# Performance work log

Measured on AMD Instinct MI355X. Metric: run time of the kernel, lower is better.

Reference implementation:

```python
import jax, jax.numpy as jnp
import numpy as np
from jax import lax

NUM_CLASSES = 9
IMG_H, IMG_W = 384, 640
SCORE_TH = 0.05
NMS_TH = 0.5
DET_PER_IMG = 100
PRE_NMS_K = 512  # pre-NMS top-k candidates per image (fixed-shape surrogate for nonzero())
BBOX_XFORM_CLIP = float(np.log(1000.0 / 16.0))
WX, WY, WW, WH = 10.0, 10.0, 5.0, 5.0
MIN_SIZE = 0.01


def _conv(x, w, padding):
    return lax.conv_general_dilated(x, w, (1, 1), padding,
                                    dimension_numbers=('NCHW', 'OIHW', 'NCHW'))


def _pairwise_iou(a, b):
    # a [K,4], b [K,4] -> [K,K]
    area_a = (a[:, 2] - a[:, 0]) * (a[:, 3] - a[:, 1])
    area_b = (b[:, 2] - b[:, 0]) * (b[:, 3] - b[:, 1])
    lt = jnp.maximum(a[:, None, :2], b[None, :, :2])
    rb = jnp.minimum(a[:, None, 2:], b[None, :, 2:])
    wh = jnp.clip(rb - lt, 0.0)
    inter = wh[..., 0] * wh[..., 1]
    return inter / jnp.maximum(area_a[:, None] + area_b[None, :] - inter, 1e-8)


def setup_inputs() -> dict:
    key = jax.random.key(0)
    ks = jax.random.split(key, 12)
    B, P, C_in = 2, 512, 512
    feats = jax.random.normal(ks[0], (B * P, C_in, 7, 7), jnp.float32)
    # well-formed proposal boxes inside the image
    cx = jax.random.uniform(ks[1], (B, P)) * IMG_W
    cy = jax.random.uniform(ks[2], (B, P)) * IMG_H
    w = jax.random.uniform(ks[3], (B, P)) * 100.0 + 8.0
    h = jax.random.uniform(ks[4], (B, P)) * 100.0 + 8.0
    proposals = jnp.stack([cx - w / 2, cy - h / 2, cx + w / 2, cy + h / 2], -1)
    w1 = jax.random.normal(ks[5], (1024, C_in, 3, 3), jnp.float32) * 0.02
    w2 = jax.random.normal(ks[6], (1024, 1024, 3, 3), jnp.float32) * 0.02
    wd = jax.random.normal(ks[7], (1024, C_in, 1, 1), jnp.float32) * 0.02
    cls_w = jax.random.normal(ks[8], (NUM_CLASSES, 1024), jnp.float32) * 0.02
    cls_b = jnp.zeros((NUM_CLASSES,), jnp.float32)
    reg_w = jax.random.normal(ks[9], (NUM_CLASSES * 4, 1024), jnp.float32) * 0.02
    reg_b = jnp.zeros((NUM_CLASSES * 4,), jnp.float32)
    return dict(instance_features=feats, proposals=proposals, w1=w1, w2=w2, wd=wd,
                cls_w=cls_w, cls_b=cls_b, reg_w=reg_w, reg_b=reg_b)


def _per_image(boxes, scores):
    # boxes [P, C, 4], scores [P, C]
    P = boxes.shape[0]
    b = boxes[:, 1:].reshape(-1, 4)                 # drop background class
    s = scores[:, 1:].reshape(-1)
    lab = jnp.broadcast_to(jnp.arange(1, NUM_CLASSES), (P, NUM_CLASSES - 1)).reshape(-1)
    ws = b[:, 2] - b[:, 0]
    hs = b[:, 3] - b[:, 1]
    valid = (s > SCORE_TH) & (ws >= MIN_SIZE) & (hs >= MIN_SIZE)
    s = jnp.where(valid, s, -jnp.inf)
    s_top, idx = lax.top_k(s, PRE_NMS_K)            # sorted descending -> greedy NMS order
    b_top = b[idx]
    lab_top = lab[idx]
    # class-aware NMS via per-class coordinate offset (batched_nms trick)
    off = lab_top.astype(b.dtype)[:, None] * (float(max(IMG_H, IMG_W)) + 1.0)
    iou = _pairwise_iou(b_top + off, b_top + off)
    keep0 = jnp.isfinite(s_top)
    ar = jnp.arange(PRE_NMS_K)

    def body(i, keep):
        sup = (iou[i] > NMS_TH) & (ar > i) & keep[i]
        return keep & ~sup

    keep = lax.fori_loop(0, PRE_NMS_K, body, keep0)
    ks = jnp.where(keep, s_top, -jnp.inf)
    fs, fidx = lax.top_k(ks, DET_PER_IMG)
    fb = b_top[fidx]
    fl = lab_top[fidx]
    fvalid = jnp.isfinite(fs)
    return (jnp.where(fvalid[:, None], fb, 0.0),
            jnp.where(fvalid, fs, 0.0),
            jnp.where(fvalid, fl, 0),
            fvalid)


def reference(instance_features, proposals, w1, w2, wd, cls_w, cls_b, reg_w, reg_b):
    B, P = proposals.shape[0], proposals.shape[1]
    x = instance_features
    # Residual_Basic: two 3x3 convs + 1x1 downsample shortcut, relu
    h = jax.nn.relu(_conv(x, w1, 'SAME'))
    h = _conv(h, w2, 'SAME')
    embedded = jax.nn.relu(h + _conv(x, wd, 'VALID'))          # [N,1024,7,7]
    flat = embedded.mean(axis=(2, 3))                          # AdaptiveAvgPool2d(1)+Flatten
    cls_scores = flat @ cls_w.T + cls_b                        # [N, C]
    bbox_reg = flat @ reg_w.T + reg_b                          # [N, 4C]

    # ---- box decode (BoxCoder weights (10,10,5,5)) ----
    props = proposals.reshape(-1, 4)
    pw = props[:, 2] - props[:, 0]
    ph = props[:, 3] - props[:, 1]
    pcx = props[:, 0] + 0.5 * pw
    pcy = props[:, 1] + 0.5 * ph
    rel = bbox_reg.reshape(-1, NUM_CLASSES, 4)
    dx = rel[..., 0] / WX
    dy = rel[..., 1] / WY
    dw = jnp.minimum(rel[..., 2] / WW, BBOX_XFORM_CLIP)
    dh = jnp.minimum(rel[..., 3] / WH, BBOX_XFORM_CLIP)
    ncx = dx * pw[:, None] + pcx[:, None]
    ncy = dy * ph[:, None] + pcy[:, None]
    nw = jnp.exp(dw) * pw[:, None]
    nh = jnp.exp(dh) * ph[:, None]
    pred_boxes = jnp.stack([ncx - 0.5 * nw, ncy - 0.5 * nh,
                            ncx + 0.5 * nw, ncy + 0.5 * nh], -1)  # [N,C,4]
    # clip to image
    pred_boxes = jnp.stack([
        jnp.clip(pred_boxes[..., 0], 0.0, IMG_W),
        jnp.clip(pred_boxes[..., 1], 0.0, IMG_H),
        jnp.clip(pred_boxes[..., 2], 0.0, IMG_W),
        jnp.clip(pred_boxes[..., 3], 0.0, IMG_H)], -1)
    pred_scores = jax.nn.softmax(cls_scores, -1)

    det_boxes, det_scores, det_labels, det_valid = jax.vmap(_per_image)(
        pred_boxes.reshape(B, P, NUM_CLASSES, 4),
        pred_scores.reshape(B, P, NUM_CLASSES))
    return embedded, cls_scores, bbox_reg, det_boxes, det_scores, det_labels, det_valid
```

## Files before the change

kernel.cpp:

```cpp
#include <hip/hip_runtime.h>
#include <math.h>

#define N_IMG 1024
#define C_IN 512
#define C_MID 1024
#define HW 7
#define SP 49
#define NCOLS (N_IMG*SP)
#define LDSROW 40

typedef short bf16x8 __attribute__((ext_vector_type(8)));
typedef float f32x4  __attribute__((ext_vector_type(4)));

__device__ __forceinline__ unsigned splitpack(float v) {
    unsigned u  = __float_as_uint(v);
    unsigned hi = (u + 0x7FFFu + ((u >> 16) & 1u)) >> 16;
    float hf    = __uint_as_float(hi << 16);
    float d     = v - hf;
    unsigned ud = __float_as_uint(d);
    unsigned lo = (ud + 0x7FFFu + ((ud >> 16) & 1u)) >> 16;
    return (hi & 0xFFFFu) | (lo << 16);
}

__global__ __launch_bounds__(256)
void pack_x(const float* __restrict__ X, unsigned* __restrict__ Xpk)
{
    int i = blockIdx.x*256 + threadIdx.x;
    Xpk[i] = splitpack(X[i]);
}

__global__ __launch_bounds__(256)
void pack_w1(const float* __restrict__ w, unsigned short* __restrict__ Wh,
             unsigned short* __restrict__ Wl)
{
    int e = blockIdx.x*256 + threadIdx.x;
    int cp = e & 31, oc = (e>>5)&127, bm = (e>>12)&7, cc = (e>>15)&15, r = e>>19;
    float v = w[((size_t)(bm*128+oc)*512 + (cc*32+cp))*9 + r];
    unsigned pk = splitpack(v);
    Wh[e] = (unsigned short)(pk & 0xFFFFu);
    Wl[e] = (unsigned short)(pk >> 16);
}
__global__ __launch_bounds__(256)
void pack_w2(const float* __restrict__ w, unsigned short* __restrict__ Wh,
             unsigned short* __restrict__ Wl)
{
    int e = blockIdx.x*256 + threadIdx.x;
    int cp = e & 31, oc = (e>>5)&127, bm = (e>>12)&7, cc = (e>>15)&31, r = e>>20;
    float v = w[((size_t)(bm*128+oc)*1024 + (cc*32+cp))*9 + r];
    unsigned pk = splitpack(v);
    Wh[e] = (unsigned short)(pk & 0xFFFFu);
    Wl[e] = (unsigned short)(pk >> 16);
}
__global__ __launch_bounds__(256)
void pack_wd(const float* __restrict__ w, unsigned short* __restrict__ Wh,
             unsigned short* __restrict__ Wl)
{
    int e = blockIdx.x*256 + threadIdx.x;
    int cp = e & 31, oc = (e>>5)&127, bm = (e>>12)&7, cc = e>>15;
    float v = w[(size_t)(bm*128+oc)*512 + cc*32+cp];
    unsigned pk = splitpack(v);
    Wh[e] = (unsigned short)(pk & 0xFFFFu);
    Wl[e] = (unsigned short)(pk >> 16);
}

template<int MODE>
__global__ __launch_bounds__(256)
void conv_mfma(const unsigned* __restrict__ Bpk,
               const float* __restrict__ Xf,
               const unsigned short* __restrict__ Wh,
               const unsigned short* __restrict__ Wl,
               const unsigned short* __restrict__ Dh,
               const unsigned short* __restrict__ Dl,
               float* __restrict__ outF, unsigned* __restrict__ outU)
{
    constexpr int CS  = MODE ? C_MID : C_IN;
    constexpr int NCC = MODE ? 32 : 16;
    __shared__ unsigned short As_hi[128*LDSROW];
    __shared__ unsigned short As_lo[128*LDSROW];
    __shared__ unsigned short Bs_hi[128*LDSROW];
    __shared__ unsigned short Bs_lo[128*LDSROW];

    const int tid = threadIdx.x;
    const int bn = blockIdx.x, bm = blockIdx.y;

    const int ln = tid & 63;
    const int wv = tid >> 6;
    const int lm = ln & 15, lq = ln >> 4;
    const int wm = (wv & 1) * 64;
    const int wn = (wv >> 1) * 64;
    const int koff = lq * 8;

    const int aoff = (tid >> 1)*LDSROW + (tid & 1)*16;
    const int bcol = tid >> 1;
    const int half16 = (tid & 1) * 16;
    const int col = bn*128 + bcol;
    const int bnimg = col / SP;
    const int bp = col - bnimg*SP;
    const int by = bp / HW;
    const int bx = bp - by*HW;
    const int bo = bcol*LDSROW + half16;

    f32x4 acc[4][4];
    #pragma unroll
    for (int i = 0; i < 4; i++)
        #pragma unroll
        for (int j = 0; j < 4; j++)
            acc[i][j] = (f32x4){0.f, 0.f, 0.f, 0.f};

    for (int r = 0; r < 9; ++r) {
        const int t3 = r / 3;
        const int dy = t3 - 1;
        const int dx = (r - t3*3) - 1;
        const bool valid = ((unsigned)(by + dy) < (unsigned)HW) &&
                           ((unsigned)(bx + dx) < (unsigned)HW);
        const int pp = bp + dy*HW + dx;
        for (int cc = 0; cc < NCC; ++cc) {
            {
                const size_t tb = ((size_t)((r*NCC + cc)*8 + bm) << 12) + tid*16;
                uint4 h0 = *(const uint4*)(Wh + tb);
                uint4 h1 = *(const uint4*)(Wh + tb + 8);
                uint4 l0 = *(const uint4*)(Wl + tb);
                uint4 l1 = *(const uint4*)(Wl + tb + 8);
                *(uint4*)&As_hi[aoff]     = h0;
                *(uint4*)&As_hi[aoff + 8] = h1;
                *(uint4*)&As_lo[aoff]     = l0;
                *(uint4*)&As_lo[aoff + 8] = l1;
            }
            {
                unsigned v[16];
                if (valid) {
                    const unsigned* src =
                        Bpk + ((size_t)bnimg*CS + cc*32 + half16)*SP + pp;
                    #pragma unroll
                    for (int e = 0; e < 16; ++e) v[e] = src[e*SP];
                } else {
                    #pragma unroll
                    for (int e = 0; e < 16; ++e) v[e] = 0u;
                }
                unsigned hp[8], lp[8];
                #pragma unroll
                for (int j2 = 0; j2 < 8; ++j2) {
                    unsigned p0 = v[2*j2], p1 = v[2*j2+1];
                    hp[j2] = (p0 & 0xFFFFu) | (p1 << 16);
                    lp[j2] = (p0 >> 16) | (p1 & 0xFFFF0000u);
                }
                *(uint4*)&Bs_hi[bo]     = *(uint4*)&hp[0];
                *(uint4*)&Bs_hi[bo + 8] = *(uint4*)&hp[4];
                *(uint4*)&Bs_lo[bo]     = *(uint4*)&lp[0];
                *(uint4*)&Bs_lo[bo + 8] = *(uint4*)&lp[4];
            }
            __syncthreads();
            {
                bf16x8 ah[4], bh[4], al[4], bl[4];
                #pragma unroll
                for (int i = 0; i < 4; i++)
                    ah[i] = *(const bf16x8*)&As_hi[(wm + i*16 + lm)*LDSROW + koff];
                #pragma unroll
                for (int j = 0; j < 4; j++)
                    bh[j] = *(const bf16x8*)&Bs_hi[(wn + j*16 + lm)*LDSROW + koff];
                #pragma unroll
                for (int i = 0; i < 4; i++)
                    #pragma unroll
                    for (int j = 0; j < 4; j++)
                        acc[i][j] = __builtin_amdgcn_mfma_f32_16x16x32_bf16(
                            ah[i], bh[j], acc[i][j], 0, 0, 0);
                #pragma unroll
                for (int i = 0; i < 4; i++)
                    al[i] = *(const bf16x8*)&As_lo[(wm + i*16 + lm)*LDSROW + koff];
                #pragma unroll
                for (int i = 0; i < 4; i++)
                    #pragma unroll
                    for (int j = 0; j < 4; j++)
                        acc[i][j] = __builtin_amdgcn_mfma_f32_16x16x32_bf16(
                            al[i], bh[j], acc[i][j], 0, 0, 0);
                #pragma unroll
                for (int j = 0; j < 4; j++)
                    bl[j] = *(const bf16x8*)&Bs_lo[(wn + j*16 + lm)*LDSROW + koff];
                #pragma unroll
                for (int i = 0; i < 4; i++)
                    #pragma unroll
                    for (int j = 0; j < 4; j++)
                        acc[i][j] = __builtin_amdgcn_mfma_f32_16x16x32_bf16(
                            ah[i], bl[j], acc[i][j], 0, 0, 0);
            }
            __syncthreads();
        }
    }
    if (MODE == 1) {
        for (int cc = 0; cc < 16; ++cc) {
            {
                const size_t tb = ((size_t)(cc*8 + bm) << 12) + tid*16;
                uint4 h0 = *(const uint4*)(Dh + tb);
                uint4 h1 = *(const uint4*)(Dh + tb + 8);
                uint4 l0 = *(const uint4*)(Dl + tb);
                uint4 l1 = *(const uint4*)(Dl + tb + 8);
                *(uint4*)&As_hi[aoff]     = h0;
                *(uint4*)&As_hi[aoff + 8] = h1;
                *(uint4*)&As_lo[aoff]     = l0;
                *(uint4*)&As_lo[aoff + 8] = l1;
            }
            {
                const float* src = Xf + ((size_t)bnimg*C_IN + cc*32 + half16)*SP + bp;
                unsigned v[16];
                #pragma unroll
                for (int e = 0; e < 16; ++e) v[e] = splitpack(src[e*SP]);
                unsigned hp[8], lp[8];
                #pragma unroll
                for (int j2 = 0; j2 < 8; ++j2) {
                    unsigned p0 = v[2*j2], p1 = v[2*j2+1];
                    hp[j2] = (p0 & 0xFFFFu) | (p1 << 16);
                    lp[j2] = (p0 >> 16) | (p1 & 0xFFFF0000u);
                }
                *(uint4*)&Bs_hi[bo]     = *(uint4*)&hp[0];
                *(uint4*)&Bs_hi[bo + 8] = *(uint4*)&hp[4];
                *(uint4*)&Bs_lo[bo]     = *(uint4*)&lp[0];
                *(uint4*)&Bs_lo[bo + 8] = *(uint4*)&lp[4];
            }
            __syncthreads();
            {
                bf16x8 ah[4], bh[4], al[4], bl[4];
                #pragma unroll
                for (int i = 0; i < 4; i++)
                    ah[i] = *(const bf16x8*)&As_hi[(wm + i*16 + lm)*LDSROW + koff];
                #pragma unroll
                for (int j = 0; j < 4; j++)
                    bh[j] = *(const bf16x8*)&Bs_hi[(wn + j*16 + lm)*LDSROW + koff];
                #pragma unroll
                for (int i = 0; i < 4; i++)
                    #pragma unroll
                    for (int j = 0; j < 4; j++)
                        acc[i][j] = __builtin_amdgcn_mfma_f32_16x16x32_bf16(
                            ah[i], bh[j], acc[i][j], 0, 0, 0);
                #pragma unroll
                for (int i = 0; i < 4; i++)
                    al[i] = *(const bf16x8*)&As_lo[(wm + i*16 + lm)*LDSROW + koff];
                #pragma unroll
                for (int i = 0; i < 4; i++)
                    #pragma unroll
                    for (int j = 0; j < 4; j++)
                        acc[i][j] = __builtin_amdgcn_mfma_f32_16x16x32_bf16(
                            al[i], bh[j], acc[i][j], 0, 0, 0);
                #pragma unroll
                for (int j = 0; j < 4; j++)
                    bl[j] = *(const bf16x8*)&Bs_lo[(wn + j*16 + lm)*LDSROW + koff];
                #pragma unroll
                for (int i = 0; i < 4; i++)
                    #pragma unroll
                    for (int j = 0; j < 4; j++)
                        acc[i][j] = __builtin_amdgcn_mfma_f32_16x16x32_bf16(
                            ah[i], bl[j], acc[i][j], 0, 0, 0);
            }
            __syncthreads();
        }
    }

    #pragma unroll
    for (int j = 0; j < 4; j++) {
        const int gc = bn*128 + wn + j*16 + lm;
        const int n = gc / SP;
        const int p = gc - n*SP;
        #pragma unroll
        for (int i = 0; i < 4; i++) {
            #pragma unroll
            for (int r = 0; r < 4; r++) {
                const int m = bm*128 + wm + i*16 + lq*4 + r;
                float val = fmaxf(acc[i][j][r], 0.f);
                if (MODE == 0)
                    outU[((size_t)n*C_MID + m)*SP + p] = splitpack(val);
                else
                    outF[((size_t)n*C_MID + m)*SP + p] = val;
            }
        }
    }
}

__global__ __launch_bounds__(256)
void pool_kernel(const float* __restrict__ emb, float* __restrict__ flat)
{
    int n = blockIdx.x;
    for (int c = threadIdx.x; c < C_MID; c += 256) {
        const float* p = emb + ((size_t)n*C_MID + c)*SP;
        float s = 0.f;
        #pragma unroll
        for (int i = 0; i < SP; i++) s += p[i];
        flat[n*C_MID + c] = s / 49.0f;
    }
}

__global__ __launch_bounds__(64)
void head_kernel(const float* __restrict__ flat,
                 const float* __restrict__ cls_w, const float* __restrict__ cls_b,
                 const float* __restrict__ reg_w, const float* __restrict__ reg_b,
                 const float* __restrict__ props,
                 float* __restrict__ cls_out, float* __restrict__ reg_out,
                 float* __restrict__ pbox, float* __restrict__ pscore)
{
    int n = blockIdx.x;
    __shared__ float f[C_MID];
    __shared__ float logits[9];
    __shared__ float regs[36];
    for (int c = threadIdx.x; c < C_MID; c += 64) f[c] = flat[n*C_MID + c];
    __syncthreads();
    int o = threadIdx.x;
    if (o < 45) {
        const float* w = (o < 9) ? (cls_w + o*C_MID) : (reg_w + (o-9)*C_MID);
        float a = (o < 9) ? cls_b[o] : reg_b[o-9];
        for (int c = 0; c < C_MID; c++) a = fmaf(f[c], w[c], a);
        if (o < 9) { cls_out[n*9 + o] = a; logits[o] = a; }
        else       { reg_out[n*36 + (o-9)] = a; regs[o-9] = a; }
    }
    __syncthreads();
    if (o < 9) {
        float m = logits[0];
        for (int i = 1; i < 9; i++) m = fmaxf(m, logits[i]);
        float se = 0.f;
        for (int i = 0; i < 9; i++) se += expf(logits[i] - m);
        pscore[n*9 + o] = expf(logits[o] - m) / se;
        {
            #pragma clang fp contract(off)
            float x1 = props[n*4+0], y1 = props[n*4+1];
            float x2 = props[n*4+2], y2 = props[n*4+3];
            float pw = x2 - x1, ph = y2 - y1;
            float pcx = x1 + 0.5f*pw, pcy = y1 + 0.5f*ph;
            float dx = regs[o*4+0] / 10.0f;
            float dy = regs[o*4+1] / 10.0f;
            float dw = fminf(regs[o*4+2] / 5.0f, 4.135166556742356f);
            float dh = fminf(regs[o*4+3] / 5.0f, 4.135166556742356f);
            float ncx = dx*pw + pcx, ncy = dy*ph + pcy;
            float nw = expf(dw)*pw,  nh = expf(dh)*ph;
            float bx1 = ncx - 0.5f*nw, by1 = ncy - 0.5f*nh;
            float bx2 = ncx + 0.5f*nw, by2 = ncy + 0.5f*nh;
            bx1 = fminf(fmaxf(bx1, 0.f), 640.f);
            by1 = fminf(fmaxf(by1, 0.f), 384.f);
            bx2 = fminf(fmaxf(bx2, 0.f), 640.f);
            by2 = fminf(fmaxf(by2, 0.f), 384.f);
            float* dst = pbox + (n*9 + o)*4;
            dst[0] = bx1; dst[1] = by1; dst[2] = bx2; dst[3] = by2;
        }
    }
}

__global__ __launch_bounds__(1024)
void nms_kernel(const float* __restrict__ pbox, const float* __restrict__ pscore,
                float* __restrict__ dbox, float* __restrict__ dsc,
                float* __restrict__ dlab, float* __restrict__ dval)
{
    #pragma clang fp contract(off)
    const int b = blockIdx.x;
    const int tid = threadIdx.x;
    __shared__ unsigned long long mbuf[4096];
    __shared__ float s512[512];
    __shared__ int   id512[512];
    __shared__ float obx[512][4];
    __shared__ unsigned long long keepw[8];
    float* sc = (float*)mbuf;
    int*   si = (int*)(sc + 4096);
    const float NEG_INF = -__builtin_inff();

    for (int i = tid; i < 4096; i += 1024) {
        int p = i >> 3;
        int c = (i & 7) + 1;
        int n = b*512 + p;
        float s = pscore[n*9 + c];
        const float* bb = pbox + (n*9 + c)*4;
        float w = bb[2] - bb[0], h = bb[3] - bb[1];
        bool valid = (s > 0.05f) && (w >= 0.01f) && (h >= 0.01f);
        sc[i] = valid ? s : NEG_INF;
        si[i] = i;
    }
    __syncthreads();
    for (int k = 2; k <= 4096; k <<= 1) {
        for (int j = k >> 1; j > 0; j >>= 1) {
            for (int i = tid; i < 4096; i += 1024) {
                int ixj = i ^ j;
                if (ixj > i) {
                    float s1 = sc[i], s2 = sc[ixj];
                    int i1 = si[i], i2 = si[ixj];
                    bool before12 = (s1 > s2) || ((s1 == s2) && (i1 < i2));
                    bool up = ((i & k) == 0);
                    if (up ? !before12 : before12) {
                        sc[i] = s2; sc[ixj] = s1;
                        si[i] = i2; si[ixj] = i1;
                    }
                }
            }
            __syncthreads();
        }
    }
    if (tid < 512) {
        float s = sc[tid];
        int id = si[tid];
        s512[tid] = s;
        id512[tid] = id;
        int c = (id & 7) + 1;
        int n = b*512 + (id >> 3);
        float off = (float)c * 641.0f;
        const float* bb = pbox + (n*9 + c)*4;
        obx[tid][0] = bb[0] + off;
        obx[tid][1] = bb[1] + off;
        obx[tid][2] = bb[2] + off;
        obx[tid][3] = bb[3] + off;
    }
    __syncthreads();
    unsigned long long* mask = mbuf;
    for (int idx = tid; idx < 4096; idx += 1024) {
        int i = idx >> 3, w = idx & 7;
        float ax1 = obx[i][0], ay1 = obx[i][1], ax2 = obx[i][2], ay2 = obx[i][3];
        float aarea = (ax2 - ax1) * (ay2 - ay1);
        unsigned long long m = 0;
        int j0 = w << 6;
        for (int jj = 0; jj < 64; jj++) {
            int j = j0 + jj;
            if (j > i) {
                float bx1 = obx[j][0], by1 = obx[j][1];
                float bx2 = obx[j][2], by2 = obx[j][3];
                float barea = (bx2 - bx1) * (by2 - by1);
                float lx = fmaxf(ax1, bx1), ly = fmaxf(ay1, by1);
                float rx = fminf(ax2, bx2), ry = fminf(ay2, by2);
                float iw = fmaxf(rx - lx, 0.f), ih = fmaxf(ry - ly, 0.f);
                float inter = iw * ih;
                float iou = inter / fmaxf(aarea + barea - inter, 1e-8f);
                if (iou > 0.5f) m |= (1ull << jj);
            }
        }
        mask[(i << 3) + w] = m;
    }
    if (tid < 8) {
        unsigned long long kw = 0;
        for (int jj = 0; jj < 64; jj++)
            if (s512[(tid << 6) + jj] != NEG_INF) kw |= (1ull << jj);
        keepw[tid] = kw;
    }
    __syncthreads();
    if (tid == 0) {
        for (int i = 0; i < 512; i++) {
            if ((keepw[i >> 6] >> (i & 63)) & 1ull) {
                const unsigned long long* mi = mask + (i << 3);
                #pragma unroll
                for (int w = 0; w < 8; w++) keepw[w] &= ~mi[w];
            }
        }
        int cnt = 0;
        for (int i = 0; i < 512 && cnt < 100; i++) {
            if ((keepw[i >> 6] >> (i & 63)) & 1ull) {
                int id = id512[i];
                int c = (id & 7) + 1;
                int n = b*512 + (id >> 3);
                const float* bb = pbox + (n*9 + c)*4;
                float* db = dbox + (b*100 + cnt)*4;
                db[0] = bb[0]; db[1] = bb[1]; db[2] = bb[2]; db[3] = bb[3];
                dsc[b*100 + cnt] = s512[i];
                dlab[b*100 + cnt] = (float)c;
                dval[b*100 + cnt] = 1.0f;
                cnt++;
            }
        }
        for (; cnt < 100; cnt++) {
            float* db = dbox + (b*100 + cnt)*4;
            db[0] = 0.f; db[1] = 0.f; db[2] = 0.f; db[3] = 0.f;
            dsc[b*100 + cnt] = 0.f;
            dlab[b*100 + cnt] = 0.f;
            dval[b*100 + cnt] = 0.f;
        }
    }
}

extern "C" void kernel_launch(void* const* d_in, const int* in_sizes, int n_in,
                              void* d_out, int out_size, void* d_ws, size_t ws_size,
                              hipStream_t stream)
{
    const float* X      = (const float*)d_in[0];
    const float* props  = (const float*)d_in[1];
    const float* w1     = (const float*)d_in[2];
    const float* w2     = (const float*)d_in[3];
    const float* wd     = (const float*)d_in[4];
    const float* cls_w  = (const float*)d_in[5];
    const float* cls_b  = (const float*)d_in[6];
    const float* reg_w  = (const float*)d_in[7];
    const float* reg_b  = (const float*)d_in[8];

    float* out     = (float*)d_out;
    float* emb     = out;
    float* cls_out = out + 51380224;
    float* reg_out = cls_out + 9216;
    float* dbox    = reg_out + 36864;
    float* dsc     = dbox + 800;
    float* dlab    = dsc + 200;
    float* dval    = dlab + 200;

    unsigned* Xpk            = (unsigned*)out;
    unsigned short* Wpk1h    = (unsigned short*)(out + 25690112);
    unsigned short* Wpk1l    = (unsigned short*)(out + 30408704);

    char* wsb = (char*)d_ws;
    unsigned* h_u         = (unsigned*)(wsb);
    unsigned short* Wpk2h = (unsigned short*)(wsb + 205520896);
    unsigned short* Wpk2l = (unsigned short*)(wsb + 224395264);
    unsigned short* Wpkdh = (unsigned short*)(wsb + 243269632);
    unsigned short* Wpkdl = (unsigned short*)(wsb + 244318208);
    float* flat           = (float*)(wsb + 245366784);
    float* pbox           = (float*)(wsb + 249561088);
    float* pscore         = (float*)(wsb + 249708544);

    pack_x <<<100352, 256, 0, stream>>>(X, Xpk);
    pack_w1<<<18432,  256, 0, stream>>>(w1, Wpk1h, Wpk1l);
    pack_w2<<<36864,  256, 0, stream>>>(w2, Wpk2h, Wpk2l);
    pack_wd<<<2048,   256, 0, stream>>>(wd, Wpkdh, Wpkdl);

    dim3 cgrid(NCOLS/128, C_MID/128);
    conv_mfma<0><<<cgrid, 256, 0, stream>>>(Xpk, X, Wpk1h, Wpk1l,
                                            nullptr, nullptr, nullptr, h_u);
    conv_mfma<1><<<cgrid, 256, 0, stream>>>(h_u, X, Wpk2h, Wpk2l,
                                            Wpkdh, Wpkdl, emb, nullptr);
    pool_kernel<<<N_IMG, 256, 0, stream>>>(emb, flat);
    head_kernel<<<N_IMG, 64, 0, stream>>>(flat, cls_w, cls_b, reg_w, reg_b, props,
                                          cls_out, reg_out, pbox, pscore);
    nms_kernel<<<2, 1024, 0, stream>>>(pbox, pscore, dbox, dsc, dlab, dval);
}
```

Before: 5.930 ms.

## Load conv weight tiles via direct global-to-LDS DMA and swap grid order

Weight tiles for the A operand are now copied straight into LDS with global_load_lds 16-byte transfers instead of going through registers. The A tile uses an unpadded 32-element row stride so the DMA layout matches. The grid is also transposed so adjacent blocks share the same column tile (the B activations) across the 8 output-channel blocks, which should improve L2 reuse of the gathered inputs. Risks: the unpadded A rows can cause LDS bank conflicts on the fragment reads, and the DMA must complete before the barrier (no explicit vmcnt wait is shown).

New measurement: 5.534 ms. 1.07x faster.

```diff
diff --git a/kernel.cpp b/kernel.cpp
--- a/kernel.cpp
+++ b/kernel.cpp
@@ -8,9 +8,16 @@
 #define SP 49
 #define NCOLS (N_IMG*SP)
 #define LDSROW 40
+#define AROW 32
 
 typedef short bf16x8 __attribute__((ext_vector_type(8)));
 typedef float f32x4  __attribute__((ext_vector_type(4)));
+
+__device__ __forceinline__ void dma16(const void* g, void* l) {
+    __builtin_amdgcn_global_load_lds(
+        (const __attribute__((address_space(1))) void*)g,
+        (__attribute__((address_space(3))) void*)l, 16, 0, 0);
+}
 
 __device__ __forceinline__ unsigned splitpack(float v) {
     unsigned u  = __float_as_uint(v);
@@ -75,13 +82,13 @@
 {
     constexpr int CS  = MODE ? C_MID : C_IN;
     constexpr int NCC = MODE ? 32 : 16;
-    __shared__ unsigned short As_hi[128*LDSROW];
-    __shared__ unsigned short As_lo[128*LDSROW];
-    __shared__ unsigned short Bs_hi[128*LDSROW];
-    __shared__ unsigned short Bs_lo[128*LDSROW];
+    __shared__ __align__(16) unsigned short As_hi[128*AROW];
+    __shared__ __align__(16) unsigned short As_lo[128*AROW];
+    __shared__ __align__(16) unsigned short Bs_hi[128*LDSROW];
+    __shared__ __align__(16) unsigned short Bs_lo[128*LDSROW];
 
     const int tid = threadIdx.x;
-    const int bn = blockIdx.x, bm = blockIdx.y;
+    const int bm = blockIdx.x, bn = blockIdx.y;
 
     const int ln = tid & 63;
     const int wv = tid >> 6;
@@ -90,7 +97,8 @@
     const int wn = (wv >> 1) * 64;
     const int koff = lq * 8;
 
-    const int aoff = (tid >> 1)*LDSROW + (tid & 1)*16;
+    const int go = wv*1024 + ln*8;
+
     const int bcol = tid >> 1;
     const int half16 = (tid & 1) * 16;
     const int col = bn*128 + bcol;
@@ -116,15 +124,11 @@
         const int pp = bp + dy*HW + dx;
         for (int cc = 0; cc < NCC; ++cc) {
             {
-                const size_t tb = ((size_t)((r*NCC + cc)*8 + bm) << 12) + tid*16;
-                uint4 h0 = *(const uint4*)(Wh + tb);
-                uint4 h1 = *(const uint4*)(Wh + tb + 8);
-                uint4 l0 = *(const uint4*)(Wl + tb);
-                uint4 l1 = *(const uint4*)(Wl + tb + 8);
-                *(uint4*)&As_hi[aoff]     = h0;
-                *(uint4*)&As_hi[aoff + 8] = h1;
-                *(uint4*)&As_lo[aoff]     = l0;
-                *(uint4*)&As_lo[aoff + 8] = l1;
+                const size_t tb = ((size_t)((r*NCC + cc)*8 + bm) << 12);
+                dma16(Wh + tb + go,       &As_hi[wv*1024]);
+                dma16(Wh + tb + go + 512, &As_hi[wv*1024 + 512]);
+                dma16(Wl + tb + go,       &As_lo[wv*1024]);
+                dma16(Wl + tb + go + 512, &As_lo[wv*1024 + 512]);
             }
             {
                 unsigned v[16];
@@ -154,7 +158,7 @@
                 bf16x8 ah[4], bh[4], al[4], bl[4];
                 #pragma unroll
                 for (int i = 0; i < 4; i++)
-                    ah[i] = *(const bf16x8*)&As_hi[(wm + i*16 + lm)*LDSROW + koff];
+                    ah[i] = *(const bf16x8*)&As_hi[(wm + i*16 + lm)*AROW + koff];
                 #pragma unroll
                 for (int j = 0; j < 4; j++)
                     bh[j] = *(const bf16x8*)&Bs_hi[(wn + j*16 + lm)*LDSROW + koff];
@@ -166,7 +170,7 @@
                             ah[i], bh[j], acc[i][j], 0, 0, 0);
                 #pragma unroll
                 for (int i = 0; i < 4; i++)
-                    al[i] = *(const bf16x8*)&As_lo[(wm + i*16 + lm)*LDSROW + koff];
+                    al[i] = *(const bf16x8*)&As_lo[(wm + i*16 + lm)*AROW + koff];
                 #pragma unroll
                 for (int i = 0; i < 4; i++)
                     #pragma unroll
@@ -189,15 +193,11 @@
     if (MODE == 1) {
         for (int cc = 0; cc < 16; ++cc) {
             {
-                const size_t tb = ((size_t)(cc*8 + bm) << 12) + tid*16;
-                uint4 h0 = *(const uint4*)(Dh + tb);
-                uint4 h1 = *(const uint4*)(Dh + tb + 8);
-                uint4 l0 = *(const uint4*)(Dl + tb);
-                uint4 l1 = *(const uint4*)(Dl + tb + 8);
-                *(uint4*)&As_hi[aoff]     = h0;
-                *(uint4*)&As_hi[aoff + 8] = h1;
-                *(uint4*)&As_lo[aoff]     = l0;
-                *(uint4*)&As_lo[aoff + 8] = l1;
+                const size_t tb = ((size_t)(cc*8 + bm) << 12);
+                dma16(Dh + tb + go,       &As_hi[wv*1024]);
+                dma16(Dh + tb + go + 512, &As_hi[wv*1024 + 512]);
+                dma16(Dl + tb + go,       &As_lo[wv*1024]);
+                dma16(Dl + tb + go + 512, &As_lo[wv*1024 + 512]);
             }
             {
                 const float* src = Xf + ((size_t)bnimg*C_IN + cc*32 + half16)*SP + bp;
@@ -221,7 +221,7 @@
                 bf16x8 ah[4], bh[4], al[4], bl[4];
                 #pragma unroll
                 for (int i = 0; i < 4; i++)
-                    ah[i] = *(const bf16x8*)&As_hi[(wm + i*16 + lm)*LDSROW + koff];
+                    ah[i] = *(const bf16x8*)&As_hi[(wm + i*16 + lm)*AROW + koff];
                 #pragma unroll
                 for (int j = 0; j < 4; j++)
                     bh[j] = *(const bf16x8*)&Bs_hi[(wn + j*16 + lm)*LDSROW + koff];
@@ -233,7 +233,7 @@
                             ah[i], bh[j], acc[i][j], 0, 0, 0);
                 #pragma unroll
                 for (int i = 0; i < 4; i++)
-                    al[i] = *(const bf16x8*)&As_lo[(wm + i*16 + lm)*LDSROW + koff];
+                    al[i] = *(const bf16x8*)&As_lo[(wm + i*16 + lm)*AROW + koff];
                 #pragma unroll
                 for (int i = 0; i < 4; i++)
                     #pragma unroll
@@ -507,7 +507,7 @@
     pack_w2<<<36864,  256, 0, stream>>>(w2, Wpk2h, Wpk2l);
     pack_wd<<<2048,   256, 0, stream>>>(wd, Wpkdh, Wpkdl);
 
-    dim3 cgrid(NCOLS/128, C_MID/128);
+    dim3 cgrid(C_MID/128, NCOLS/128);
     conv_mfma<0><<<cgrid, 256, 0, stream>>>(Xpk, X, Wpk1h, Wpk1l,
                                             nullptr, nullptr, nullptr, h_u);
     conv_mfma<1><<<cgrid, 256, 0, stream>>>(h_u, X, Wpk2h, Wpk2l,
```
